# Performance work log

Hardware: AMD Instinct MI355X
Metric: run time of the kernel (lower is better)

The kernel has to match this reference:

```python
import jax, jax.numpy as jnp
import numpy as np

# ---- sizes ----
N_ATOM = 23   # NUMBER_ATOMIC_GRAPH_FEATURES
N_BOND = 7    # NUMBER_BOND_GRAPH_FEATURES
N_NODES = 50000
N_EDGES = 400000
N_MOLS = 2000  # 25 atoms per molecule

# irreps as lists of (mul, l, parity)
IRR_SH    = [(1, 0, 1), (1, 1, -1), (1, 2, 1)]            # 1x0e+1x1o+1x2e, dim 9
IRR_ATOMS = [(N_ATOM, 0, 1)]                               # 23x0e
IRR_MID1  = [(16,0,1),(6,1,1),(6,1,-1),(4,2,1),(4,2,-1)]  # dim 92
IRR_MID2  = [(8,0,1),(3,1,1),(3,1,-1),(2,2,1),(4,2,-1)]   # dim 56
IRR_OUT   = [(1, 0, 1)]                                    # 0e

# ---- real Wigner 3j via null space of rotation-generator constraints ----

def _su2_J(l):
    m = np.arange(-l, l + 1)
    Jz = np.diag(m).astype(complex)
    jp = np.zeros((2*l+1, 2*l+1), complex)
    for i, mm in enumerate(m[:-1]):
        jp[i+1, i] = np.sqrt(l*(l+1) - mm*(mm+1))
    jm = jp.conj().T
    return (jp + jm) / 2, (jp - jm) / 2j, Jz


def _c2r(l):
    # complex -> real spherical-harmonic change of basis (rows: real m'=-l..l)
    d = 2*l + 1
    Q = np.zeros((d, d), complex)
    Q[l, l] = 1.0
    s2 = np.sqrt(2.0)
    for m in range(1, l + 1):
        Q[l+m, l+m] = (-1)**m / s2
        Q[l+m, l-m] = 1.0 / s2
        Q[l-m, l-m] = 1j / s2
        Q[l-m, l+m] = -1j * (-1)**m / s2
    return Q


def _real_gens(l):
    Q = _c2r(l)
    return [np.real(Q @ (-1j*J) @ Q.conj().T) for J in _su2_J(l)]

_W3J = {}

def w3j(l1, l2, l3):
    key = (l1, l2, l3)
    if key not in _W3J:
        K1, K2, K3 = _real_gens(l1), _real_gens(l2), _real_gens(l3)
        d1, d2, d3 = 2*l1+1, 2*l2+1, 2*l3+1
        I1, I2, I3 = np.eye(d1), np.eye(d2), np.eye(d3)
        rows = []
        for a in range(3):
            rows.append(np.kron(np.kron(K1[a], I2), I3)
                        + np.kron(np.kron(I1, K2[a]), I3)
                        + np.kron(np.kron(I1, I2), K3[a]))
        _, _, vh = np.linalg.svd(np.concatenate(rows, 0))
        v = vh[-1]
        v = v / np.linalg.norm(v)
        v = v * np.sign(v[np.argmax(np.abs(v))])  # fix sign convention
        _W3J[key] = v.reshape(d1, d2, d3).astype(np.float32)
    return _W3J[key]

# ---- spherical harmonics lmax=2, component normalization, normalize=False ----

def _sh(v):
    x, y, z = v[:, 0], v[:, 1], v[:, 2]
    r2 = x*x + y*y + z*z
    s3, s5, s15 = np.sqrt(3.0), np.sqrt(5.0), np.sqrt(15.0)
    return jnp.stack([
        jnp.ones_like(x),                     # l=0
        s3*y, s3*z, s3*x,                     # l=1 (m=-1,0,1)
        s15*x*y, s15*y*z, 0.5*s5*(3*z*z - r2), s15*x*z, 0.5*s15*(x*x - y*y),  # l=2
    ], axis=-1)

# ---- fully connected tensor product (e3nn-style, component norm) ----

def _slices(irr):
    out, off = [], 0
    for (mul, l, _p) in irr:
        out.append((off, mul, 2*l + 1))
        off += mul * (2*l + 1)
    return out


def _paths(irr1, irr2, irr3):
    ps = []
    for i1, (m1, l1, p1) in enumerate(irr1):
        for i2, (m2, l2, p2) in enumerate(irr2):
            for i3, (m3, l3, p3) in enumerate(irr3):
                if p1 * p2 == p3 and abs(l1 - l2) <= l3 <= l1 + l2:
                    ps.append((i1, i2, i3))
    return ps


def fc_numel(irr1, irr2, irr3):
    return sum(irr1[i1][0]*irr2[i2][0]*irr3[i3][0] for i1, i2, i3 in _paths(irr1, irr2, irr3))


def fc_tp(x1, x2, irr1, irr2, irr3, wflat):
    s1, s2, s3 = _slices(irr1), _slices(irr2), _slices(irr3)
    ps = _paths(irr1, irr2, irr3)
    fan = {}
    for i1, i2, i3 in ps:
        fan[i3] = fan.get(i3, 0) + irr1[i1][0] * irr2[i2][0]
    E = x1.shape[0]
    chunks = [jnp.zeros((E, m*(2*l+1)), x1.dtype) for (m, l, _p) in irr3]
    off = 0
    for i1, i2, i3 in ps:
        (o1, m1, d1), (o2, m2, d2), (o3, m3, d3) = s1[i1], s2[i2], s3[i3]
        n = m1 * m2 * m3
        W = wflat[off:off+n].reshape(m1, m2, m3); off += n
        a = x1[:, o1:o1+m1*d1].reshape(E, m1, d1)
        b = x2[:, o2:o2+m2*d2].reshape(E, m2, d2)
        C = jnp.asarray(w3j((d1-1)//2, (d2-1)//2, (d3-1)//2))
        pw = float(np.sqrt(d3 / fan[i3]))  # component-norm path weight
        chunks[i3] = chunks[i3] + pw * jnp.einsum('ijk,eui,evj,uvw->ewk', C, a, b, W).reshape(E, -1)
    return jnp.concatenate(chunks, axis=-1)

# ---- model ----

def setup_inputs() -> dict:
    key = jax.random.key(0)
    ks = jax.random.split(key, 10)
    positions = jax.random.normal(ks[0], (N_NODES, 3), jnp.float32) * 3.0
    x = jax.random.uniform(ks[1], (N_NODES, N_ATOM), jnp.float32)
    edge_attr = jax.random.uniform(ks[2], (N_EDGES, N_BOND), jnp.float32)
    edge_src = jax.random.randint(ks[3], (N_EDGES,), 0, N_NODES)
    # ensure every node has >= 1 incoming edge (matches torch degree()/div semantics)
    edge_dst = jnp.concatenate([jnp.arange(N_NODES),
                                jax.random.randint(ks[4], (N_EDGES - N_NODES,), 0, N_NODES)])
    batch = jnp.repeat(jnp.arange(N_MOLS), N_NODES // N_MOLS)
    lin_w = jax.random.normal(ks[5], (N_ATOM, N_ATOM), jnp.float32) / np.sqrt(N_ATOM)
    lin_b = jax.random.normal(ks[6], (N_ATOM,), jnp.float32) * 0.1
    w_tp1 = jax.random.normal(ks[7], (fc_numel(IRR_ATOMS, IRR_SH, IRR_MID1),), jnp.float32)
    w_tp2 = jax.random.normal(ks[8], (fc_numel(IRR_MID1, IRR_SH, IRR_MID2),), jnp.float32)
    w_tp3 = jax.random.normal(ks[9], (fc_numel(IRR_MID2, IRR_SH, IRR_OUT),), jnp.float32)
    return dict(positions=positions, x=x, edge_attr=edge_attr, lin_w=lin_w, lin_b=lin_b,
                w_tp1=w_tp1, w_tp2=w_tp2, w_tp3=w_tp3,
                edge_src=edge_src, edge_dst=edge_dst, batch=batch)


def reference(positions, x, edge_attr, lin_w, lin_b, w_tp1, w_tp2, w_tp3,
              edge_src, edge_dst, batch):
    edge_vec = positions[edge_src] - positions[edge_dst]           # [E,3]
    sh = _sh(edge_vec)                                             # [E,9]
    # mul_edges: uvu (no weights), only in1 slot 0 used -> first bond scalar times each sh irrep
    eattr = edge_attr[:, 0:1] * sh                                 # [E,9]
    ones_e = jnp.ones((N_EDGES,), positions.dtype)
    deg = jax.ops.segment_sum(ones_e, edge_dst, num_segments=N_NODES)
    dis = 1.0 / jnp.sqrt(deg)                                      # every node covered
    first = jax.nn.relu(x[edge_src] @ lin_w.T + lin_b)             # [E,23]
    ef = fc_tp(first, eattr, IRR_ATOMS, IRR_SH, IRR_MID1, w_tp1)   # [E,92]
    nf = jax.ops.segment_sum(ef, edge_dst, num_segments=N_NODES) * dis[:, None]
    ef = fc_tp(nf[edge_src], eattr, IRR_MID1, IRR_SH, IRR_MID2, w_tp2)  # [E,56]
    nf = jax.ops.segment_sum(ef, edge_dst, num_segments=N_NODES) * dis[:, None]
    ef = fc_tp(nf[edge_src], eattr, IRR_MID2, IRR_SH, IRR_OUT, w_tp3)   # [E,1]
    nf = jax.ops.segment_sum(ef, edge_dst, num_segments=N_NODES) * dis[:, None]
    acc = jax.ops.segment_sum(nf, batch, num_segments=N_MOLS)      # [M,1]
    apm = jax.ops.segment_sum(jnp.ones((N_NODES,), positions.dtype), batch, num_segments=N_MOLS)
    return acc / jnp.sqrt(apm)[:, None]
```

## Files before the change

### kernel.cpp

```cpp
#include <hip/hip_runtime.h>

#define NNODES 50000
#define NEDGES 400000
#define NMOLS  2000
#define NBLK   196

constexpr size_t OFF_CNT   = 0;
constexpr size_t OFF_OFFS  = 50000;
constexpr size_t OFF_CURS  = 100000;
constexpr size_t OFF_BSUM  = 150000;
constexpr size_t OFF_SRCS  = 150256;
constexpr size_t OFF_EB4   = 550256;
constexpr size_t OFF_GB    = 2150256;
constexpr size_t OFF_AB    = 2950256;
constexpr size_t OFF_TB    = 4550256;
constexpr size_t OFF_HH    = 8550256;

__device__ __forceinline__ unsigned short f2bf(float f) {
  unsigned int b = __float_as_uint(f);
  unsigned int r = (b + 0x7FFFu + ((b >> 16) & 1u)) >> 16;
  return (unsigned short)r;
}
__device__ __forceinline__ float bflo(unsigned int u) { return __uint_as_float(u << 16); }
__device__ __forceinline__ float bfhi(unsigned int u) { return __uint_as_float(u & 0xFFFF0000u); }
__device__ __forceinline__ unsigned int packbf(float a, float b) {
  return (unsigned int)f2bf(a) | ((unsigned int)f2bf(b) << 16);
}

__device__ __forceinline__ void make_b(float w0, float dx, float dy, float dz, float* b) {
  const float s3 = 1.7320508075688772f, s5c = 2.2360679774997896f, s15 = 3.872983346207417f;
  float r2 = dx * dx + dy * dy + dz * dz;
  b[0] = w0;
  b[1] = w0 * s3 * dy;
  b[2] = w0 * s3 * dz;
  b[3] = w0 * s3 * dx;
  b[4] = w0 * s15 * dx * dy;
  b[5] = w0 * s15 * dy * dz;
  b[6] = w0 * 0.5f * s5c * (3.f * dz * dz - r2);
  b[7] = w0 * s15 * dx * dz;
  b[8] = w0 * 0.5f * s15 * (dx * dx - dy * dy);
}

#define TU(i) ((((i) & 3) == 0) ? Qv[(i) >> 2].x : (((i) & 3) == 1) ? Qv[(i) >> 2].y \
             : (((i) & 3) == 2) ? Qv[(i) >> 2].z : Qv[(i) >> 2].w)

__global__ void k_count(const int* __restrict__ dst, int* __restrict__ cnt) {
  int e = blockIdx.x * blockDim.x + threadIdx.x;
  if (e < NEDGES) atomicAdd(cnt + dst[e], 1);
}

__global__ void k_scanA(const int* __restrict__ cnt, int* __restrict__ offs, int* __restrict__ bsum) {
  __shared__ int sh[256];
  int t = threadIdx.x, i = blockIdx.x * 256 + t;
  int c = (i < NNODES) ? cnt[i] : 0;
  sh[t] = c; __syncthreads();
  #pragma unroll
  for (int off = 1; off < 256; off <<= 1) {
    int v = (t >= off) ? sh[t - off] : 0; __syncthreads();
    sh[t] += v; __syncthreads();
  }
  if (i < NNODES) offs[i] = sh[t] - c;
  if (t == 255) bsum[blockIdx.x] = sh[255];
}

__global__ void k_scanB(int* __restrict__ bsum) {
  __shared__ int sh[256];
  int t = threadIdx.x;
  int v = (t < NBLK) ? bsum[t] : 0;
  sh[t] = v; __syncthreads();
  #pragma unroll
  for (int off = 1; off < 256; off <<= 1) {
    int u = (t >= off) ? sh[t - off] : 0; __syncthreads();
    sh[t] += u; __syncthreads();
  }
  bsum[t] = sh[t] - v;
}

__global__ void k_scanC(int* __restrict__ offs, int* __restrict__ curs, const int* __restrict__ bsum) {
  int i = blockIdx.x * 256 + threadIdx.x;
  if (i < NNODES) {
    int o = offs[i] + bsum[blockIdx.x];
    offs[i] = o;
    curs[i] = o;
  }
}

__global__ void k_fill(const float* __restrict__ pos, const float* __restrict__ ea,
                       const int* __restrict__ src, const int* __restrict__ dst,
                       int* __restrict__ curs, int* __restrict__ srcs, float4* __restrict__ eb4) {
  int e = blockIdx.x * blockDim.x + threadIdx.x;
  if (e >= NEDGES) return;
  int s = src[e], d = dst[e];
  int p = atomicAdd(curs + d, 1);
  srcs[p] = s;
  float dx = pos[3 * s] - pos[3 * d];
  float dy = pos[3 * s + 1] - pos[3 * d + 1];
  float dz = pos[3 * s + 2] - pos[3 * d + 2];
  eb4[p] = make_float4(dx, dy, dz, ea[(size_t)e * 7]);
}

__global__ void __launch_bounds__(256, 2)
k_node1(const float* __restrict__ x, const float* __restrict__ lw,
        const float* __restrict__ lb, const float* __restrict__ w1,
        unsigned int* __restrict__ gb) {
  int n = blockIdx.x * blockDim.x + threadIdx.x;
  if (n >= NNODES) return;
  float f[23];
  const float* xr = x + (size_t)n * 23;
  #pragma unroll
  for (int v = 0; v < 23; ++v) {
    float acc = lb[v];
    const float* wr = lw + v * 23;
    #pragma unroll
    for (int c = 0; c < 23; ++c) acc += xr[c] * wr[c];
    f[v] = fmaxf(acc, 0.f);
  }
  float G[26];
  #pragma unroll
  for (int w = 0; w < 16; ++w) { float a = 0; for (int v = 0; v < 23; ++v) a += f[v] * w1[v * 16 + w]; G[w] = a; }
  #pragma unroll
  for (int w = 0; w < 6;  ++w) { float a = 0; for (int v = 0; v < 23; ++v) a += f[v] * w1[368 + v * 6 + w]; G[16 + w] = a; }
  #pragma unroll
  for (int w = 0; w < 4;  ++w) { float a = 0; for (int v = 0; v < 23; ++v) a += f[v] * w1[506 + v * 4 + w]; G[22 + w] = a; }
  unsigned int U[16];
  #pragma unroll
  for (int i = 0; i < 13; ++i) U[i] = packbf(G[2 * i], G[2 * i + 1]);
  U[13] = U[14] = U[15] = 0u;
  uint4* o = (uint4*)(gb + (size_t)n * 16);
  o[0] = make_uint4(U[0], U[1], U[2], U[3]);
  o[1] = make_uint4(U[4], U[5], U[6], U[7]);
  o[2] = make_uint4(U[8], U[9], U[10], U[11]);
  o[3] = make_uint4(U[12], U[13], U[14], U[15]);
}

__global__ void __launch_bounds__(256, 2)
k_gather1(const int* __restrict__ offs, const int* __restrict__ cnt,
          const int* __restrict__ srcs, const float4* __restrict__ eb4,
          const unsigned int* __restrict__ gb, unsigned int* __restrict__ ab) {
  int tid = blockIdx.x * 256 + threadIdx.x;
  int n = tid >> 3, sl = tid & 7;
  if (n >= NNODES) return;
  int beg = offs[n], cn = cnt[n];
  float M[54];
  #pragma unroll
  for (int i = 0; i < 54; ++i) M[i] = 0.f;
  for (int j = sl; j < cn; j += 8) {
    int p = beg + j;
    int s = srcs[p];
    float4 ebv = eb4[p];
    float bb[9]; make_b(ebv.w, ebv.x, ebv.y, ebv.z, bb);
    const uint4* Gf = (const uint4*)(gb + (size_t)s * 16);
    uint4 u0 = Gf[0], u1 = Gf[1], u2 = Gf[2], u3 = Gf[3];
    unsigned int U[13] = { u0.x, u0.y, u0.z, u0.w, u1.x, u1.y, u1.z, u1.w,
                           u2.x, u2.y, u2.z, u2.w, u3.x };
    #pragma unroll
    for (int u = 0; u < 16; ++u) {
      float gv = (u & 1) ? bfhi(U[u >> 1]) : bflo(U[u >> 1]);
      M[u] += bb[0] * gv;
    }
    #pragma unroll
    for (int u = 0; u < 6; ++u) {
      int idx = 16 + u;
      float gv = (idx & 1) ? bfhi(U[idx >> 1]) : bflo(U[idx >> 1]);
      #pragma unroll
      for (int k = 0; k < 3; ++k) M[16 + 3 * u + k] += bb[1 + k] * gv;
    }
    #pragma unroll
    for (int u = 0; u < 4; ++u) {
      int idx = 22 + u;
      float gv = (idx & 1) ? bfhi(U[idx >> 1]) : bflo(U[idx >> 1]);
      #pragma unroll
      for (int K = 0; K < 5; ++K) M[34 + 5 * u + K] += bb[4 + K] * gv;
    }
  }
  #pragma unroll
  for (int m = 1; m < 8; m <<= 1)
    #pragma unroll
    for (int i = 0; i < 54; ++i) M[i] += __shfl_xor(M[i], m);
  if (sl == 0) {
    const float S23 = 0.20851441405707477f;
    float sc = S23 * rsqrtf((float)cn);
    unsigned int U[32];
    #pragma unroll
    for (int i = 0; i < 27; ++i) U[i] = packbf(sc * M[2 * i], sc * M[2 * i + 1]);
    #pragma unroll
    for (int i = 27; i < 32; ++i) U[i] = 0u;
    uint4* o4 = (uint4*)(ab + (size_t)n * 32);
    #pragma unroll
    for (int q = 0; q < 8; ++q)
      o4[q] = make_uint4(U[4 * q], U[4 * q + 1], U[4 * q + 2], U[4 * q + 3]);
  }
}

__global__ void __launch_bounds__(256, 2)
k_node2t(const unsigned int* __restrict__ ab, const float* __restrict__ w2,
         unsigned int* __restrict__ tb) {
  __shared__ float W[596];
  for (int i = threadIdx.x; i < 596; i += 256) W[i] = w2[i];
  __syncthreads();
  int n = blockIdx.x * 256 + threadIdx.x;
  if (n >= NNODES) return;
  float A[54];
  {
    const uint4* Af = (const uint4*)(ab + (size_t)n * 32);
    uint4 q0 = Af[0], q1 = Af[1], q2 = Af[2], q3 = Af[3], q4 = Af[4], q5 = Af[5], q6 = Af[6];
    unsigned int U[27] = { q0.x, q0.y, q0.z, q0.w, q1.x, q1.y, q1.z, q1.w,
                           q2.x, q2.y, q2.z, q2.w, q3.x, q3.y, q3.z, q3.w,
                           q4.x, q4.y, q4.z, q4.w, q5.x, q5.y, q5.z, q5.w,
                           q6.x, q6.y, q6.z };
    #pragma unroll
    for (int i = 0; i < 27; ++i) { A[2 * i] = bflo(U[i]); A[2 * i + 1] = bfhi(U[i]); }
  }

  unsigned int U[72];
  #pragma unroll
  for (int w = 0; w < 8; ++w) {
    float s0 = 0;
    #pragma unroll
    for (int u = 0; u < 16; ++u) s0 += A[u] * W[u * 8 + w];
    float p2[3];
    #pragma unroll
    for (int k = 0; k < 3; ++k) { float s = 0; for (int u = 0; u < 6; ++u) s += A[16 + 3 * u + k] * W[316 + 8 * u + w]; p2[k] = s; }
    float q3[5];
    #pragma unroll
    for (int K = 0; K < 5; ++K) { float s = 0; for (int u = 0; u < 4; ++u) s += A[34 + 5 * u + K] * W[472 + 8 * u + w]; q3[K] = s; }
    U[5 * w + 0] = packbf(s0, p2[0]);
    U[5 * w + 1] = packbf(p2[1], p2[2]);
    U[5 * w + 2] = packbf(q3[0], q3[1]);
    U[5 * w + 3] = packbf(q3[2], q3[3]);
    U[5 * w + 4] = packbf(q3[4], 0.f);
  }
  #pragma unroll
  for (int w = 0; w < 3; ++w) {
    float s1 = 0;
    #pragma unroll
    for (int u = 0; u < 16; ++u) s1 += A[u] * W[128 + 3 * u + w];
    float p1[3], p4[3];
    #pragma unroll
    for (int k = 0; k < 3; ++k) {
      float a = 0, c = 0;
      #pragma unroll
      for (int u = 0; u < 6; ++u) {
        a += A[16 + 3 * u + k] * W[298 + 3 * u + w];
        c += A[16 + 3 * u + k] * W[394 + 3 * u + w];
      }
      p1[k] = a; p4[k] = c;
    }
    float q2[5];
    #pragma unroll
    for (int K = 0; K < 5; ++K) { float s = 0; for (int u = 0; u < 4; ++u) s += A[34 + 5 * u + K] * W[444 + 3 * u + w]; q2[K] = s; }
    int base = 40 + 6 * w;
    U[base + 0] = packbf(s1, p1[0]);
    U[base + 1] = packbf(p1[1], p1[2]);
    U[base + 2] = packbf(p4[0], p4[1]);
    U[base + 3] = packbf(p4[2], q2[0]);
    U[base + 4] = packbf(q2[1], q2[2]);
    U[base + 5] = packbf(q2[3], q2[4]);
  }
  #pragma unroll
  for (int w = 0; w < 2; ++w) {
    float s2 = 0;
    #pragma unroll
    for (int u = 0; u < 16; ++u) s2 += A[u] * W[176 + 2 * u + w];
    float q1[5], q4[5];
    #pragma unroll
    for (int K = 0; K < 5; ++K) {
      float a = 0, c = 0;
      #pragma unroll
      for (int u = 0; u < 4; ++u) {
        a += A[34 + 5 * u + K] * W[436 + 2 * u + w];
        c += A[34 + 5 * u + K] * W[516 + 2 * u + w];
      }
      q1[K] = a; q4[K] = c;
    }
    float p3[3];
    #pragma unroll
    for (int k = 0; k < 3; ++k) { float s = 0; for (int u = 0; u < 6; ++u) s += A[16 + 3 * u + k] * W[382 + 2 * u + w]; p3[k] = s; }
    int base = 58 + 7 * w;
    U[base + 0] = packbf(s2, q1[0]);
    U[base + 1] = packbf(q1[1], q1[2]);
    U[base + 2] = packbf(q1[3], q1[4]);
    U[base + 3] = packbf(p3[0], p3[1]);
    U[base + 4] = packbf(p3[2], q4[0]);
    U[base + 5] = packbf(q4[1], q4[2]);
    U[base + 6] = packbf(q4[3], q4[4]);
  }
  uint4* o = (uint4*)(tb + (size_t)n * 80);
  #pragma unroll
  for (int q = 0; q < 18; ++q)
    o[q] = make_uint4(U[4 * q], U[4 * q + 1], U[4 * q + 2], U[4 * q + 3]);
}

__global__ void __launch_bounds__(256, 2)
k_edge2c(const int* __restrict__ offs, const int* __restrict__ cnt,
         const int* __restrict__ srcs, const float4* __restrict__ eb4,
         const unsigned int* __restrict__ tb, const float* __restrict__ w3,
         float* __restrict__ hh) {
  int tid = blockIdx.x * 256 + threadIdx.x;
  int n = tid >> 3, sl = tid & 7;
  if (n >= NNODES) return;
  int beg = offs[n], cn = cnt[n];
  float O0[8], O2[9], O3[10];
  #pragma unroll
  for (int i = 0; i < 8; ++i) O0[i] = 0.f;
  #pragma unroll
  for (int i = 0; i < 9; ++i) O2[i] = 0.f;
  #pragma unroll
  for (int i = 0; i < 10; ++i) O3[i] = 0.f;

  const float I3 = 0.5773502691896258f, I5 = 0.4472135954999579f;
  const float CA = 0.18257418583505536f, CB = 0.31622776601683794f, CC = 0.3651483716701107f;
  const float P = 0.2390457218668787f, Q = 0.2070196678027063f, R = 0.1195228609334394f;

  for (int j = sl; j < cn; j += 8) {
    int p = beg + j;
    int s = srcs[p];
    const uint4* T4 = (const uint4*)(tb + (size_t)s * 80);
    uint4 Qv[18];
    #pragma unroll
    for (int i = 0; i < 18; ++i) Qv[i] = T4[i];
    float4 ebv = eb4[p];
    float b[9]; make_b(ebv.w, ebv.x, ebv.y, ebv.z, b);

    #pragma unroll
    for (int w = 0; w < 8; ++w) {
      unsigned int u0 = TU(5 * w), u1 = TU(5 * w + 1), u2 = TU(5 * w + 2),
                   u3 = TU(5 * w + 3), u4 = TU(5 * w + 4);
      O0[w] += b[0] * bflo(u0)
             + I3 * (bfhi(u0) * b[1] + bflo(u1) * b[2] + bfhi(u1) * b[3])
             + I5 * (bflo(u2) * b[4] + bfhi(u2) * b[5] + bflo(u3) * b[6]
                   + bfhi(u3) * b[7] + bflo(u4) * b[8]);
    }
    #pragma unroll
    for (int w = 0; w < 3; ++w) {
      unsigned int u0 = TU(40 + 6 * w), u1 = TU(41 + 6 * w), u2 = TU(42 + 6 * w),
                   u3 = TU(43 + 6 * w), u4 = TU(44 + 6 * w), u5 = TU(45 + 6 * w);
      float ta  = bflo(u0);
      float tb0 = bfhi(u0), tb1 = bflo(u1), tb2 = bfhi(u1);
      float tc0 = bflo(u2), tc1 = bfhi(u2), tc2 = bflo(u3);
      float td0 = bfhi(u3), td1 = bflo(u4), td2 = bfhi(u4), td3 = bflo(u5), td4 = bfhi(u5);
      O2[3 * w + 0] += I3 * (b[1] * ta + b[0] * tb0)
                     + tc0 * (-CA * b[6] - CB * b[8]) + tc1 * (CB * b[5]) + tc2 * (CB * b[4])
                     + td0 * (CB * b[3]) + td1 * (CB * b[2]) - td2 * (CA * b[1]) - td4 * (CB * b[1]);
      O2[3 * w + 1] += I3 * (b[2] * ta + b[0] * tb1)
                     + tc0 * (CB * b[5]) + tc1 * (CC * b[6]) + tc2 * (CB * b[7])
                     + td1 * (CB * b[1]) + td2 * (CC * b[2]) + td3 * (CB * b[3]);
      O2[3 * w + 2] += I3 * (b[3] * ta + b[0] * tb2)
                     + tc0 * (CB * b[4]) + tc1 * (CB * b[7]) + tc2 * (-CA * b[6] + CB * b[8])
                     + td0 * (CB * b[1]) - td2 * (CA * b[3]) + td3 * (CB * b[2]) + td4 * (CB * b[3]);
    }
    #pragma unroll
    for (int w = 0; w < 2; ++w) {
      unsigned int u0 = TU(58 + 7 * w), u1 = TU(59 + 7 * w), u2 = TU(60 + 7 * w),
                   u3 = TU(61 + 7 * w), u4 = TU(62 + 7 * w), u5 = TU(63 + 7 * w),
                   u6 = TU(64 + 7 * w);
      float ta  = bflo(u0);
      float tb0 = bfhi(u0), tb1 = bflo(u1), tb2 = bfhi(u1), tb3 = bflo(u2), tb4 = bfhi(u2);
      float tc0 = bflo(u3), tc1 = bfhi(u3), tc2 = bflo(u4);
      float td0 = bfhi(u4), td1 = bflo(u5), td2 = bfhi(u5), td3 = bflo(u6), td4 = bfhi(u6);
      O3[5 * w + 0] += I5 * (b[4] * ta + b[0] * tb0)
                     + tc0 * (CB * b[3]) + tc2 * (CB * b[1])
                     - (P * b[6]) * td0 + (Q * b[7]) * td1 - (P * b[4]) * td2 + (Q * b[5]) * td3;
      O3[5 * w + 1] += I5 * (b[5] * ta + b[0] * tb1)
                     + tc0 * (CB * b[2]) + tc1 * (CB * b[1])
                     + (Q * b[7]) * td0 + (R * b[6] - Q * b[8]) * td1 + (R * b[5]) * td2
                     + (Q * b[4]) * td3 - (Q * b[5]) * td4;
      O3[5 * w + 2] += I5 * (b[6] * ta + b[0] * tb2)
                     - tc0 * (CA * b[1]) + tc1 * (CC * b[2]) - tc2 * (CA * b[3])
                     - (P * b[4]) * td0 + (R * b[5]) * td1 + (P * b[6]) * td2
                     + (R * b[7]) * td3 - (P * b[8]) * td4;
      O3[5 * w + 3] += I5 * (b[7] * ta + b[0] * tb3)
                     + tc1 * (CB * b[3]) + tc2 * (CB * b[2])
                     + (Q * b[5]) * td0 + (Q * b[4]) * td1 + (R * b[7]) * td2
                     + (R * b[6] + Q * b[8]) * td3 + (Q * b[7]) * td4;
      O3[5 * w + 4] += I5 * (b[8] * ta + b[0] * tb4)
                     - tc0 * (CB * b[1]) + tc2 * (CB * b[3])
                     - (Q * b[5]) * td1 - (P * b[8]) * td2 + (Q * b[7]) * td3 - (P * b[6]) * td4;
    }
  }

  #pragma unroll
  for (int m = 1; m < 8; m <<= 1) {
    #pragma unroll
    for (int i = 0; i < 8; ++i) O0[i] += __shfl_xor(O0[i], m);
    #pragma unroll
    for (int i = 0; i < 9; ++i) O2[i] += __shfl_xor(O2[i], m);
    #pragma unroll
    for (int i = 0; i < 10; ++i) O3[i] += __shfl_xor(O3[i], m);
  }

  if (sl == 0) {
    const float S26 = 0.19611613513818404f, S14 = 0.2672612419124244f, S8 = 0.35355339059327373f;
    const float S13 = 0.2773500981126146f;
    float di = rsqrtf((float)cn);
    float F[27];
    #pragma unroll
    for (int w = 0; w < 8; ++w) F[w] = S26 * di * O0[w];
    #pragma unroll
    for (int i = 0; i < 9; ++i) F[8 + i] = S14 * di * O2[i];
    #pragma unroll
    for (int i = 0; i < 10; ++i) F[17 + i] = S8 * di * O3[i];

    float h[9];
    float t0 = 0;
    #pragma unroll
    for (int u = 0; u < 8; ++u) t0 += F[u] * w3[u];
    h[0] = S13 * t0;
    #pragma unroll
    for (int jj = 0; jj < 3; ++jj) {
      float s1 = 0;
      #pragma unroll
      for (int u = 0; u < 3; ++u) s1 += F[8 + 3 * u + jj] * w3[8 + u];
      h[1 + jj] = S13 * I3 * s1;
    }
    #pragma unroll
    for (int K = 0; K < 5; ++K)
      h[4 + K] = S13 * I5 * (F[17 + K] * w3[11] + F[22 + K] * w3[12]);

    float4* o4 = (float4*)(hh + (size_t)n * 16);
    o4[0] = make_float4(h[0], h[1], h[2], h[3]);
    o4[1] = make_float4(h[4], h[5], h[6], h[7]);
    o4[2] = make_float4(h[8], 0.f, 0.f, 0.f);
  }
}

__global__ void k_gather3(const int* __restrict__ offs, const int* __restrict__ cnt,
                          const int* __restrict__ srcs, const float4* __restrict__ eb4,
                          const float* __restrict__ hh, const int* __restrict__ batch,
                          float* __restrict__ out) {
  int tid = blockIdx.x * 256 + threadIdx.x;
  int n = tid >> 3, sl = tid & 7;
  if (n >= NNODES) return;
  int beg = offs[n], cn = cnt[n];
  float v = 0.f;
  for (int j = sl; j < cn; j += 8) {
    int p = beg + j;
    int s = srcs[p];
    float4 ebv = eb4[p];
    float b[9]; make_b(ebv.w, ebv.x, ebv.y, ebv.z, b);
    const float4* Hf = (const float4*)(hh + (size_t)s * 16);
    float4 hA = Hf[0], hB = Hf[1];
    float h8 = Hf[2].x;
    v += b[0] * hA.x + b[1] * hA.y + b[2] * hA.z + b[3] * hA.w
       + b[4] * hB.x + b[5] * hB.y + b[6] * hB.z + b[7] * hB.w
       + b[8] * h8;
  }
  #pragma unroll
  for (int m = 1; m < 8; m <<= 1) v += __shfl_xor(v, m);
  if (sl == 0) {
    float di = rsqrtf((float)cn);
    unsafeAtomicAdd(out + batch[n], v * di * 0.2f);
  }
}

extern "C" void kernel_launch(void* const* d_in, const int* in_sizes, int n_in,
                              void* d_out, int out_size, void* d_ws, size_t ws_size,
                              hipStream_t stream) {
  const float* positions = (const float*)d_in[0];
  const float* x         = (const float*)d_in[1];
  const float* edge_attr = (const float*)d_in[2];
  const float* lin_w     = (const float*)d_in[3];
  const float* lin_b     = (const float*)d_in[4];
  const float* w_tp1     = (const float*)d_in[5];
  const float* w_tp2     = (const float*)d_in[6];
  const float* w_tp3     = (const float*)d_in[7];
  const int*   edge_src  = (const int*)d_in[8];
  const int*   edge_dst  = (const int*)d_in[9];
  const int*   batch     = (const int*)d_in[10];
  float* out = (float*)d_out;

  int*   cnt  = (int*)d_ws + OFF_CNT;
  int*   offs = (int*)d_ws + OFF_OFFS;
  int*   curs = (int*)d_ws + OFF_CURS;
  int*   bsum = (int*)d_ws + OFF_BSUM;
  int*   srcs = (int*)d_ws + OFF_SRCS;
  float4* eb4 = (float4*)((float*)d_ws + OFF_EB4);
  unsigned int* gb = (unsigned int*)((float*)d_ws + OFF_GB);
  unsigned int* ab = (unsigned int*)((float*)d_ws + OFF_AB);
  unsigned int* tb = (unsigned int*)((float*)d_ws + OFF_TB);
  float* hh   = (float*)d_ws + OFF_HH;

  hipMemsetAsync(cnt, 0, NNODES * sizeof(int), stream);
  hipMemsetAsync(out, 0, (size_t)out_size * sizeof(float), stream);

  dim3 blk256(256);
  dim3 gEdge((NEDGES + 255) / 256);
  dim3 gNode256((NNODES + 255) / 256);
  dim3 gCoop((NNODES * 8 + 255) / 256);

  k_count<<<gEdge, blk256, 0, stream>>>(edge_dst, cnt);
  k_scanA<<<dim3(NBLK), blk256, 0, stream>>>(cnt, offs, bsum);
  k_scanB<<<dim3(1), blk256, 0, stream>>>(bsum);
  k_scanC<<<dim3(NBLK), blk256, 0, stream>>>(offs, curs, bsum);
  k_fill<<<gEdge, blk256, 0, stream>>>(positions, edge_attr, edge_src, edge_dst, curs, srcs, eb4);
  k_node1<<<gNode256, blk256, 0, stream>>>(x, lin_w, lin_b, w_tp1, gb);
  k_gather1<<<gCoop, blk256, 0, stream>>>(offs, cnt, srcs, eb4, gb, ab);
  k_node2t<<<gNode256, blk256, 0, stream>>>(ab, w_tp2, tb);
  k_edge2c<<<gCoop, blk256, 0, stream>>>(offs, cnt, srcs, eb4, tb, w_tp3, hh);
  k_gather3<<<gCoop, blk256, 0, stream>>>(offs, cnt, srcs, eb4, hh, batch, out);
}
```

Before: 165.5 us.

## Fuse node-2 transform into gather and fold memsets into node-1 prep kernel

Merges the gather of layer-1 messages with the layer-2 per-node weight transform. After the shuffle reduction, each of the 8 lanes computes a slice of the output channels straight from registers, which removes the bf16 intermediate buffer write and read and one kernel launch. A second change folds the two memsets into the first node kernel, which now runs first and zeroes the counters and output. In exchange, the intermediate is no longer rounded to bf16, the tb stores become scattered 32-bit writes instead of uint4 stores, and lanes do uneven work.

```diff
diff --git a/kernel.cpp b/kernel.cpp
--- a/kernel.cpp
+++ b/kernel.cpp
@@ -12,9 +12,8 @@
 constexpr size_t OFF_SRCS  = 150256;
 constexpr size_t OFF_EB4   = 550256;
 constexpr size_t OFF_GB    = 2150256;
-constexpr size_t OFF_AB    = 2950256;
-constexpr size_t OFF_TB    = 4550256;
-constexpr size_t OFF_HH    = 8550256;
+constexpr size_t OFF_TB    = 2950256;
+constexpr size_t OFF_HH    = 6950256;
 
 __device__ __forceinline__ unsigned short f2bf(float f) {
   unsigned int b = __float_as_uint(f);
@@ -44,6 +43,43 @@
 #define TU(i) ((((i) & 3) == 0) ? Qv[(i) >> 2].x : (((i) & 3) == 1) ? Qv[(i) >> 2].y \
              : (((i) & 3) == 2) ? Qv[(i) >> 2].z : Qv[(i) >> 2].w)
 
+__global__ void __launch_bounds__(256, 2)
+k_prep(const float* __restrict__ x, const float* __restrict__ lw,
+       const float* __restrict__ lb, const float* __restrict__ w1,
+       unsigned int* __restrict__ gb, int* __restrict__ cnt,
+       float* __restrict__ out, int out_n) {
+  int n = blockIdx.x * blockDim.x + threadIdx.x;
+  if (n < NNODES) cnt[n] = 0;
+  if (n < out_n) out[n] = 0.f;
+  if (n >= NNODES) return;
+  float f[23];
+  const float* xr = x + (size_t)n * 23;
+  #pragma unroll
+  for (int v = 0; v < 23; ++v) {
+    float acc = lb[v];
+    const float* wr = lw + v * 23;
+    #pragma unroll
+    for (int c = 0; c < 23; ++c) acc += xr[c] * wr[c];
+    f[v] = fmaxf(acc, 0.f);
+  }
+  float G[26];
+  #pragma unroll
+  for (int w = 0; w < 16; ++w) { float a = 0; for (int v = 0; v < 23; ++v) a += f[v] * w1[v * 16 + w]; G[w] = a; }
+  #pragma unroll
+  for (int w = 0; w < 6;  ++w) { float a = 0; for (int v = 0; v < 23; ++v) a += f[v] * w1[368 + v * 6 + w]; G[16 + w] = a; }
+  #pragma unroll
+  for (int w = 0; w < 4;  ++w) { float a = 0; for (int v = 0; v < 23; ++v) a += f[v] * w1[506 + v * 4 + w]; G[22 + w] = a; }
+  unsigned int U[16];
+  #pragma unroll
+  for (int i = 0; i < 13; ++i) U[i] = packbf(G[2 * i], G[2 * i + 1]);
+  U[13] = U[14] = U[15] = 0u;
+  uint4* o = (uint4*)(gb + (size_t)n * 16);
+  o[0] = make_uint4(U[0], U[1], U[2], U[3]);
+  o[1] = make_uint4(U[4], U[5], U[6], U[7]);
+  o[2] = make_uint4(U[8], U[9], U[10], U[11]);
+  o[3] = make_uint4(U[12], U[13], U[14], U[15]);
+}
+
 __global__ void k_count(const int* __restrict__ dst, int* __restrict__ cnt) {
   int e = blockIdx.x * blockDim.x + threadIdx.x;
   if (e < NEDGES) atomicAdd(cnt + dst[e], 1);
@@ -100,43 +136,13 @@
 }
 
 __global__ void __launch_bounds__(256, 2)
-k_node1(const float* __restrict__ x, const float* __restrict__ lw,
-        const float* __restrict__ lb, const float* __restrict__ w1,
-        unsigned int* __restrict__ gb) {
-  int n = blockIdx.x * blockDim.x + threadIdx.x;
-  if (n >= NNODES) return;
-  float f[23];
-  const float* xr = x + (size_t)n * 23;
-  #pragma unroll
-  for (int v = 0; v < 23; ++v) {
-    float acc = lb[v];
-    const float* wr = lw + v * 23;
-    #pragma unroll
-    for (int c = 0; c < 23; ++c) acc += xr[c] * wr[c];
-    f[v] = fmaxf(acc, 0.f);
-  }
-  float G[26];
-  #pragma unroll
-  for (int w = 0; w < 16; ++w) { float a = 0; for (int v = 0; v < 23; ++v) a += f[v] * w1[v * 16 + w]; G[w] = a; }
-  #pragma unroll
-  for (int w = 0; w < 6;  ++w) { float a = 0; for (int v = 0; v < 23; ++v) a += f[v] * w1[368 + v * 6 + w]; G[16 + w] = a; }
-  #pragma unroll
-  for (int w = 0; w < 4;  ++w) { float a = 0; for (int v = 0; v < 23; ++v) a += f[v] * w1[506 + v * 4 + w]; G[22 + w] = a; }
-  unsigned int U[16];
-  #pragma unroll
-  for (int i = 0; i < 13; ++i) U[i] = packbf(G[2 * i], G[2 * i + 1]);
-  U[13] = U[14] = U[15] = 0u;
-  uint4* o = (uint4*)(gb + (size_t)n * 16);
-  o[0] = make_uint4(U[0], U[1], U[2], U[3]);
-  o[1] = make_uint4(U[4], U[5], U[6], U[7]);
-  o[2] = make_uint4(U[8], U[9], U[10], U[11]);
-  o[3] = make_uint4(U[12], U[13], U[14], U[15]);
-}
-
-__global__ void __launch_bounds__(256, 2)
-k_gather1(const int* __restrict__ offs, const int* __restrict__ cnt,
-          const int* __restrict__ srcs, const float4* __restrict__ eb4,
-          const unsigned int* __restrict__ gb, unsigned int* __restrict__ ab) {
+k_gather1t(const int* __restrict__ offs, const int* __restrict__ cnt,
+           const int* __restrict__ srcs, const float4* __restrict__ eb4,
+           const unsigned int* __restrict__ gb, const float* __restrict__ w2,
+           unsigned int* __restrict__ tb) {
+  __shared__ float W[596];
+  for (int i = threadIdx.x; i < 596; i += 256) W[i] = w2[i];
+  __syncthreads();
   int tid = blockIdx.x * 256 + threadIdx.x;
   int n = tid >> 3, sl = tid & 7;
   if (n >= NNODES) return;
@@ -177,118 +183,84 @@
   for (int m = 1; m < 8; m <<= 1)
     #pragma unroll
     for (int i = 0; i < 54; ++i) M[i] += __shfl_xor(M[i], m);
-  if (sl == 0) {
-    const float S23 = 0.20851441405707477f;
-    float sc = S23 * rsqrtf((float)cn);
-    unsigned int U[32];
-    #pragma unroll
-    for (int i = 0; i < 27; ++i) U[i] = packbf(sc * M[2 * i], sc * M[2 * i + 1]);
-    #pragma unroll
-    for (int i = 27; i < 32; ++i) U[i] = 0u;
-    uint4* o4 = (uint4*)(ab + (size_t)n * 32);
-    #pragma unroll
-    for (int q = 0; q < 8; ++q)
-      o4[q] = make_uint4(U[4 * q], U[4 * q + 1], U[4 * q + 2], U[4 * q + 3]);
-  }
-}
-
-__global__ void __launch_bounds__(256, 2)
-k_node2t(const unsigned int* __restrict__ ab, const float* __restrict__ w2,
-         unsigned int* __restrict__ tb) {
-  __shared__ float W[596];
-  for (int i = threadIdx.x; i < 596; i += 256) W[i] = w2[i];
-  __syncthreads();
-  int n = blockIdx.x * 256 + threadIdx.x;
-  if (n >= NNODES) return;
-  float A[54];
+
+  const float S23 = 0.20851441405707477f;
+  float sc = S23 * rsqrtf((float)cn);
+  #pragma unroll
+  for (int i = 0; i < 54; ++i) M[i] *= sc;
+
+  unsigned int* trow = tb + (size_t)n * 80;
   {
-    const uint4* Af = (const uint4*)(ab + (size_t)n * 32);
-    uint4 q0 = Af[0], q1 = Af[1], q2 = Af[2], q3 = Af[3], q4 = Af[4], q5 = Af[5], q6 = Af[6];
-    unsigned int U[27] = { q0.x, q0.y, q0.z, q0.w, q1.x, q1.y, q1.z, q1.w,
-                           q2.x, q2.y, q2.z, q2.w, q3.x, q3.y, q3.z, q3.w,
-                           q4.x, q4.y, q4.z, q4.w, q5.x, q5.y, q5.z, q5.w,
-                           q6.x, q6.y, q6.z };
-    #pragma unroll
-    for (int i = 0; i < 27; ++i) { A[2 * i] = bflo(U[i]); A[2 * i + 1] = bfhi(U[i]); }
-  }
-
-  unsigned int U[72];
-  #pragma unroll
-  for (int w = 0; w < 8; ++w) {
+    int w = sl;
     float s0 = 0;
     #pragma unroll
-    for (int u = 0; u < 16; ++u) s0 += A[u] * W[u * 8 + w];
+    for (int u = 0; u < 16; ++u) s0 += M[u] * W[u * 8 + w];
     float p2[3];
     #pragma unroll
-    for (int k = 0; k < 3; ++k) { float s = 0; for (int u = 0; u < 6; ++u) s += A[16 + 3 * u + k] * W[316 + 8 * u + w]; p2[k] = s; }
+    for (int k = 0; k < 3; ++k) { float s = 0; for (int u = 0; u < 6; ++u) s += M[16 + 3 * u + k] * W[316 + 8 * u + w]; p2[k] = s; }
     float q3[5];
     #pragma unroll
-    for (int K = 0; K < 5; ++K) { float s = 0; for (int u = 0; u < 4; ++u) s += A[34 + 5 * u + K] * W[472 + 8 * u + w]; q3[K] = s; }
-    U[5 * w + 0] = packbf(s0, p2[0]);
-    U[5 * w + 1] = packbf(p2[1], p2[2]);
-    U[5 * w + 2] = packbf(q3[0], q3[1]);
-    U[5 * w + 3] = packbf(q3[2], q3[3]);
-    U[5 * w + 4] = packbf(q3[4], 0.f);
-  }
-  #pragma unroll
-  for (int w = 0; w < 3; ++w) {
+    for (int K = 0; K < 5; ++K) { float s = 0; for (int u = 0; u < 4; ++u) s += M[34 + 5 * u + K] * W[472 + 8 * u + w]; q3[K] = s; }
+    trow[5 * w + 0] = packbf(s0, p2[0]);
+    trow[5 * w + 1] = packbf(p2[1], p2[2]);
+    trow[5 * w + 2] = packbf(q3[0], q3[1]);
+    trow[5 * w + 3] = packbf(q3[2], q3[3]);
+    trow[5 * w + 4] = packbf(q3[4], 0.f);
+  }
+  if (sl < 3) {
+    int w = sl;
     float s1 = 0;
     #pragma unroll
-    for (int u = 0; u < 16; ++u) s1 += A[u] * W[128 + 3 * u + w];
+    for (int u = 0; u < 16; ++u) s1 += M[u] * W[128 + 3 * u + w];
     float p1[3], p4[3];
     #pragma unroll
     for (int k = 0; k < 3; ++k) {
       float a = 0, c = 0;
       #pragma unroll
       for (int u = 0; u < 6; ++u) {
-        a += A[16 + 3 * u + k] * W[298 + 3 * u + w];
-        c += A[16 + 3 * u + k] * W[394 + 3 * u + w];
+        a += M[16 + 3 * u + k] * W[298 + 3 * u + w];
+        c += M[16 + 3 * u + k] * W[394 + 3 * u + w];
       }
       p1[k] = a; p4[k] = c;
     }
     float q2[5];
     #pragma unroll
-    for (int K = 0; K < 5; ++K) { float s = 0; for (int u = 0; u < 4; ++u) s += A[34 + 5 * u + K] * W[444 + 3 * u + w]; q2[K] = s; }
+    for (int K = 0; K < 5; ++K) { float s = 0; for (int u = 0; u < 4; ++u) s += M[34 + 5 * u + K] * W[444 + 3 * u + w]; q2[K] = s; }
     int base = 40 + 6 * w;
-    U[base + 0] = packbf(s1, p1[0]);
-    U[base + 1] = packbf(p1[1], p1[2]);
-    U[base + 2] = packbf(p4[0], p4[1]);
-    U[base + 3] = packbf(p4[2], q2[0]);
-    U[base + 4] = packbf(q2[1], q2[2]);
-    U[base + 5] = packbf(q2[3], q2[4]);
-  }
-  #pragma unroll
-  for (int w = 0; w < 2; ++w) {
+    trow[base + 0] = packbf(s1, p1[0]);
+    trow[base + 1] = packbf(p1[1], p1[2]);
+    trow[base + 2] = packbf(p4[0], p4[1]);
+    trow[base + 3] = packbf(p4[2], q2[0]);
+    trow[base + 4] = packbf(q2[1], q2[2]);
+    trow[base + 5] = packbf(q2[3], q2[4]);
+  } else if (sl < 5) {
+    int w = sl - 3;
     float s2 = 0;
     #pragma unroll
-    for (int u = 0; u < 16; ++u) s2 += A[u] * W[176 + 2 * u + w];
+    for (int u = 0; u < 16; ++u) s2 += M[u] * W[176 + 2 * u + w];
     float q1[5], q4[5];
     #pragma unroll
     for (int K = 0; K < 5; ++K) {
       float a = 0, c = 0;
       #pragma unroll
       for (int u = 0; u < 4; ++u) {
-        a += A[34 + 5 * u + K] * W[436 + 2 * u + w];
-        c += A[34 + 5 * u + K] * W[516 + 2 * u + w];
+        a += M[34 + 5 * u + K] * W[436 + 2 * u + w];
+        c += M[34 + 5 * u + K] * W[516 + 2 * u + w];
       }
       q1[K] = a; q4[K] = c;
     }
     float p3[3];
     #pragma unroll
-    for (int k = 0; k < 3; ++k) { float s = 0; for (int u = 0; u < 6; ++u) s += A[16 + 3 * u + k] * W[382 + 2 * u + w]; p3[k] = s; }
+    for (int k = 0; k < 3; ++k) { float s = 0; for (int u = 0; u < 6; ++u) s += M[16 + 3 * u + k] * W[382 + 2 * u + w]; p3[k] = s; }
     int base = 58 + 7 * w;
-    U[base + 0] = packbf(s2, q1[0]);
-    U[base + 1] = packbf(q1[1], q1[2]);
-    U[base + 2] = packbf(q1[3], q1[4]);
-    U[base + 3] = packbf(p3[0], p3[1]);
-    U[base + 4] = packbf(p3[2], q4[0]);
-    U[base + 5] = packbf(q4[1], q4[2]);
-    U[base + 6] = packbf(q4[3], q4[4]);
-  }
-  uint4* o = (uint4*)(tb + (size_t)n * 80);
-  #pragma unroll
-  for (int q = 0; q < 18; ++q)
-    o[q] = make_uint4(U[4 * q], U[4 * q + 1], U[4 * q + 2], U[4 * q + 3]);
+    trow[base + 0] = packbf(s2, q1[0]);
+    trow[base + 1] = packbf(q1[1], q1[2]);
+    trow[base + 2] = packbf(q1[3], q1[4]);
+    trow[base + 3] = packbf(p3[0], p3[1]);
+    trow[base + 4] = packbf(p3[2], q4[0]);
+    trow[base + 5] = packbf(q4[1], q4[2]);
+    trow[base + 6] = packbf(q4[3], q4[4]);
+  }
 }
 
 __global__ void __launch_bounds__(256, 2)
@@ -476,26 +448,21 @@
   int*   srcs = (int*)d_ws + OFF_SRCS;
   float4* eb4 = (float4*)((float*)d_ws + OFF_EB4);
   unsigned int* gb = (unsigned int*)((float*)d_ws + OFF_GB);
-  unsigned int* ab = (unsigned int*)((float*)d_ws + OFF_AB);
   unsigned int* tb = (unsigned int*)((float*)d_ws + OFF_TB);
   float* hh   = (float*)d_ws + OFF_HH;
-
-  hipMemsetAsync(cnt, 0, NNODES * sizeof(int), stream);
-  hipMemsetAsync(out, 0, (size_t)out_size * sizeof(float), stream);
 
   dim3 blk256(256);
   dim3 gEdge((NEDGES + 255) / 256);
   dim3 gNode256((NNODES + 255) / 256);
   dim3 gCoop((NNODES * 8 + 255) / 256);
 
+  k_prep<<<gNode256, blk256, 0, stream>>>(x, lin_w, lin_b, w_tp1, gb, cnt, out, out_size);
   k_count<<<gEdge, blk256, 0, stream>>>(edge_dst, cnt);
   k_scanA<<<dim3(NBLK), blk256, 0, stream>>>(cnt, offs, bsum);
   k_scanB<<<dim3(1), blk256, 0, stream>>>(bsum);
   k_scanC<<<dim3(NBLK), blk256, 0, stream>>>(offs, curs, bsum);
   k_fill<<<gEdge, blk256, 0, stream>>>(positions, edge_attr, edge_src, edge_dst, curs, srcs, eb4);
-  k_node1<<<gNode256, blk256, 0, stream>>>(x, lin_w, lin_b, w_tp1, gb);
-  k_gather1<<<gCoop, blk256, 0, stream>>>(offs, cnt, srcs, eb4, gb, ab);
-  k_node2t<<<gNode256, blk256, 0, stream>>>(ab, w_tp2, tb);
+  k_gather1t<<<gCoop, blk256, 0, stream>>>(offs, cnt, srcs, eb4, gb, w_tp2, tb);
   k_edge2c<<<gCoop, blk256, 0, stream>>>(offs, cnt, srcs, eb4, tb, w_tp3, hh);
   k_gather3<<<gCoop, blk256, 0, stream>>>(offs, cnt, srcs, eb4, hh, batch, out);
 }
```

After: 150.6 us. 1.1x faster.
